# Performance work log

Measured on AMD Instinct MI355X. Metric: run time of the kernel, lower is better.

The kernel has to match this reference:

```python
import jax, jax.numpy as jnp
import numpy as np

DEPTH = 6
HEADS = 8
DIM = 512
DH = DIM // HEADS          # 64
SEQ = 512
BATCH = 8
MEM = 4096                 # KNN memory slots per batch element (scaled from 64000)
TOPK = 32                  # num_retrieved_memories
KNN_LAYERS = (3, 4)        # memorizing_layers=(4,5), 1-indexed -> 0-indexed 3,4
FF = 4 * DIM


def setup_inputs() -> dict:
    key = jax.random.key(0)
    ks = jax.random.split(key, 18)
    s = 0.02
    return {
        "x":     jax.random.normal(ks[0], (BATCH, SEQ, DIM), jnp.float32),
        "Wq":    jax.random.normal(ks[1], (DEPTH, DIM, DIM), jnp.float32) * s,
        "Wk":    jax.random.normal(ks[2], (DEPTH, DIM, DIM), jnp.float32) * s,
        "Wv":    jax.random.normal(ks[3], (DEPTH, DIM, DIM), jnp.float32) * s,
        "Wo":    jax.random.normal(ks[4], (DEPTH, DIM, DIM), jnp.float32) * s,
        "ln1_s": jnp.ones((DEPTH, DIM), jnp.float32),
        "ln1_b": jnp.zeros((DEPTH, DIM), jnp.float32),
        "ln2_s": jnp.ones((DEPTH, DIM), jnp.float32),
        "ln2_b": jnp.zeros((DEPTH, DIM), jnp.float32),
        "W1":    jax.random.normal(ks[5], (DEPTH, DIM, FF), jnp.float32) * s,
        "W2":    jax.random.normal(ks[6], (DEPTH, FF, DIM), jnp.float32) * s,
        "lnf_s": jnp.ones((DIM,), jnp.float32),
        "lnf_b": jnp.zeros((DIM,), jnp.float32),
        # pre-populated KNN memory banks (keys/values in head dim), one per memorizing layer
        "mem_k": jax.random.normal(ks[7], (len(KNN_LAYERS), BATCH, MEM, DH), jnp.float32),
        "mem_v": jax.random.normal(ks[8], (len(KNN_LAYERS), BATCH, MEM, DH), jnp.float32),
    }


def _ln(x, s, b):
    m = x.mean(-1, keepdims=True)
    v = ((x - m) ** 2).mean(-1, keepdims=True)
    return (x - m) * jax.lax.rsqrt(v + 1e-5) * s + b


def _gather_mem(mem, idx):
    # mem: (b, M, d), idx: (b, h, n, K) -> (b, h, n, K, d)
    return jax.vmap(lambda m, i: m[i])(mem, idx)


def reference(x, Wq, Wk, Wv, Wo, ln1_s, ln1_b, ln2_s, ln2_b, W1, W2,
              lnf_s, lnf_b, mem_k, mem_v):
    b, n, d = x.shape
    scale = DH ** -0.5
    causal = jnp.tril(jnp.ones((n, n), dtype=bool))
    neg = jnp.float32(-1e9)
    mem_i = 0
    for l in range(DEPTH):
        h = _ln(x, ln1_s[l], ln1_b[l])
        q = (h @ Wq[l]).reshape(b, n, HEADS, DH)
        k = (h @ Wk[l]).reshape(b, n, HEADS, DH)
        v = (h @ Wv[l]).reshape(b, n, HEADS, DH)
        sim = jnp.einsum('bihd,bjhd->bhij', q, k) * scale
        sim = jnp.where(causal, sim, neg)
        if l in KNN_LAYERS:
            mk, mv = mem_k[mem_i], mem_v[mem_i]              # (b, M, dh)
            # KNN search: dense scoring + top-k retrieval
            sim_all = jnp.einsum('bihd,bmd->bhim', q, mk) * scale  # (b,h,n,M)
            top_sim, top_idx = jax.lax.top_k(sim_all, TOPK)        # (b,h,n,K)
            gv = _gather_mem(mv, top_idx)                          # (b,h,n,K,dh)
            # joint softmax over [retrieved memories, local causal]
            logits = jnp.concatenate([top_sim, sim], axis=-1)
            attn = jax.nn.softmax(logits, axis=-1)
            a_mem, a_loc = attn[..., :TOPK], attn[..., TOPK:]
            out = (jnp.einsum('bhik,bhikd->bhid', a_mem, gv)
                   + jnp.einsum('bhij,bjhd->bhid', a_loc, v))
            mem_i += 1
        else:
            attn = jax.nn.softmax(sim, axis=-1)
            out = jnp.einsum('bhij,bjhd->bhid', attn, v)
        out = out.transpose(0, 2, 1, 3).reshape(b, n, d) @ Wo[l]
        x = x + out
        h2 = _ln(x, ln2_s[l], ln2_b[l])
        x = x + jax.nn.gelu(h2 @ W1[l]) @ W2[l]
    return _ln(x, lnf_s, lnf_b)
```

## Files before the change

kernel.cpp:

```cpp
#include <hip/hip_runtime.h>
#include <math.h>

#define BB 8
#define NN 512
#define DD 512
#define HH 8
#define DHH 64
#define FFF 2048
#define MEMM 4096
#define TOPKK 32
#define DEPTHH 6
#define NT (BB*NN)
#define QKVS 1536

typedef __bf16 bf16x8 __attribute__((ext_vector_type(8)));
typedef __bf16 bf16x4 __attribute__((ext_vector_type(4)));
typedef float f32x4 __attribute__((ext_vector_type(4)));

template <int OBF16>
__global__ __launch_bounds__(256) void ln_kernel(const float* __restrict__ xin,
                                                 const float* __restrict__ g,
                                                 const float* __restrict__ bt,
                                                 void* __restrict__ outv) {
  __shared__ float red[4];
  int tok = blockIdx.x;
  const float* xr = xin + (size_t)tok * DD;
  int t = threadIdx.x;
  float v0 = xr[t], v1 = xr[t + 256];
  float s = v0 + v1;
#pragma unroll
  for (int m = 32; m; m >>= 1) s += __shfl_xor(s, m, 64);
  if ((t & 63) == 0) red[t >> 6] = s;
  __syncthreads();
  float mean = (red[0] + red[1] + red[2] + red[3]) * (1.0f / 512.0f);
  float d0 = v0 - mean, d1 = v1 - mean;
  float vv = d0 * d0 + d1 * d1;
#pragma unroll
  for (int m = 32; m; m >>= 1) vv += __shfl_xor(vv, m, 64);
  __syncthreads();
  if ((t & 63) == 0) red[t >> 6] = vv;
  __syncthreads();
  float var = (red[0] + red[1] + red[2] + red[3]) * (1.0f / 512.0f);
  float inv = rsqrtf(var + 1e-5f);
  float o0 = d0 * inv * g[t] + bt[t];
  float o1 = d1 * inv * g[t + 256] + bt[t + 256];
  if (OBF16) {
    __bf16* out = (__bf16*)outv;
    out[(size_t)tok * DD + t] = (__bf16)o0;
    out[(size_t)tok * DD + t + 256] = (__bf16)o1;
  } else {
    float* out = (float*)outv;
    out[(size_t)tok * DD + t] = o0;
    out[(size_t)tok * DD + t + 256] = o1;
  }
}

__device__ inline float gelu_f(float x) {
  float x3 = x * x * x;
  return 0.5f * x * (1.0f + tanhf(0.7978845608028654f * (x + 0.044715f * x3)));
}

__global__ __launch_bounds__(256) void transpose_all_kernel(
    const float* __restrict__ Wq, const float* __restrict__ Wk,
    const float* __restrict__ Wv, const float* __restrict__ Wo,
    const float* __restrict__ W1, const float* __restrict__ W2,
    __bf16* __restrict__ wqT, __bf16* __restrict__ wkT,
    __bf16* __restrict__ wvT, __bf16* __restrict__ woT,
    __bf16* __restrict__ w1T, __bf16* __restrict__ w2T) {
  __shared__ float tile[32][33];
  int tid = blockIdx.x;
  const float* src; __bf16* dst; int K, N, tt;
  if (tid < 1024) {
    int which = tid >> 8; tt = tid & 255; K = 512; N = 512;
    src = (which == 0) ? Wq : (which == 1) ? Wk : (which == 2) ? Wv : Wo;
    dst = (which == 0) ? wqT : (which == 1) ? wkT : (which == 2) ? wvT : woT;
  } else if (tid < 2048) {
    tt = tid - 1024; K = 512; N = 2048; src = W1; dst = w1T;
  } else {
    tt = tid - 2048; K = 2048; N = 512; src = W2; dst = w2T;
  }
  int nx = N >> 5;
  int n0 = (tt % nx) * 32, k0 = (tt / nx) * 32;
  int tx = threadIdx.x & 31, ty = threadIdx.x >> 5;
#pragma unroll
  for (int i = 0; i < 4; i++) {
    int r = ty + i * 8;
    tile[r][tx] = src[(size_t)(k0 + r) * N + n0 + tx];
  }
  __syncthreads();
#pragma unroll
  for (int i = 0; i < 4; i++) {
    int r = ty + i * 8;
    dst[(size_t)(n0 + r) * K + k0 + tx] = (__bf16)tile[tx][r];
  }
}

__device__ __forceinline__ void gload16(const __bf16* g, __bf16* lds) {
  __builtin_amdgcn_global_load_lds(
      (const __attribute__((address_space(1))) void*)g,
      (__attribute__((address_space(3))) void*)lds, 16, 0, 0);
}

template <int EPI, int OBF16>
__global__ __launch_bounds__(256) void gemm_mfma128(const __bf16* __restrict__ A,
                                                    const __bf16* __restrict__ Bt,
                                                    const float* __restrict__ R,
                                                    void* __restrict__ Cout,
                                                    int M, int N, int K) {
  __shared__ __align__(16) __bf16 Als[128 * 64];
  __shared__ __align__(16) __bf16 Bls[128 * 64];
  int t = threadIdx.x;
  int bn = blockIdx.x, bm = blockIdx.y;
  int lane = t & 63, w = t >> 6;
  int wr = w >> 1, wc = w & 1;
  int m15 = lane & 15, q = lane >> 4;
  f32x4 acc[4][4] = {};
  for (int kt = 0; kt < K; kt += 64) {
    __syncthreads();
#pragma unroll
    for (int i = 0; i < 4; i++) {
      int rg = w * 32 + i * 8;
      int row = rg + (lane >> 3);
      int lcol = (lane & 7) * 8;
      gload16(A + (size_t)(bm * 128 + row) * K + kt + lcol, &Als[rg * 64]);
      gload16(Bt + (size_t)(bn * 128 + row) * K + kt + lcol, &Bls[rg * 64]);
    }
    __syncthreads();
#pragma unroll
    for (int ks = 0; ks < 2; ks++) {
      bf16x8 af[4], bfr[4];
#pragma unroll
      for (int mt = 0; mt < 4; mt++)
        af[mt] = *(const bf16x8*)&Als[(wr * 64 + mt * 16 + m15) * 64 + (ks * 4 + q) * 8];
#pragma unroll
      for (int nt = 0; nt < 4; nt++)
        bfr[nt] = *(const bf16x8*)&Bls[(wc * 64 + nt * 16 + m15) * 64 + (ks * 4 + q) * 8];
#pragma unroll
      for (int mt = 0; mt < 4; mt++)
#pragma unroll
        for (int nt = 0; nt < 4; nt++)
          acc[mt][nt] = __builtin_amdgcn_mfma_f32_16x16x32_bf16(af[mt], bfr[nt],
                                                                acc[mt][nt], 0, 0, 0);
    }
  }
#pragma unroll
  for (int mt = 0; mt < 4; mt++) {
#pragma unroll
    for (int nt = 0; nt < 4; nt++) {
      int gc = bn * 128 + wc * 64 + nt * 16 + m15;
#pragma unroll
      for (int r = 0; r < 4; r++) {
        int gr = bm * 128 + wr * 64 + mt * 16 + q * 4 + r;
        size_t off = (size_t)gr * N + gc;
        float v = acc[mt][nt][r];
        if (EPI == 1) v = gelu_f(v);
        if (EPI == 2) v += R[off];
        if (OBF16) ((__bf16*)Cout)[off] = (__bf16)v;
        else       ((float*)Cout)[off] = v;
      }
    }
  }
}

template <int EPI, int OBF16>
__global__ __launch_bounds__(256) void gemm_mfma64(const __bf16* __restrict__ A,
                                                   const __bf16* __restrict__ Bt,
                                                   const float* __restrict__ R,
                                                   void* __restrict__ Cout,
                                                   int M, int N, int K) {
  __shared__ __align__(16) __bf16 Als[128 * 64];
  __shared__ __align__(16) __bf16 Bls[64 * 64];
  int t = threadIdx.x;
  int bn = blockIdx.x, bm = blockIdx.y;
  int lane = t & 63, w = t >> 6;
  int wr = w >> 1, wc = w & 1;
  int m15 = lane & 15, q = lane >> 4;
  f32x4 acc[4][2] = {};
  for (int kt = 0; kt < K; kt += 64) {
    __syncthreads();
#pragma unroll
    for (int i = 0; i < 4; i++) {
      int rg = w * 32 + i * 8;
      int row = rg + (lane >> 3);
      int lcol = (lane & 7) * 8;
      gload16(A + (size_t)(bm * 128 + row) * K + kt + lcol, &Als[rg * 64]);
    }
#pragma unroll
    for (int i = 0; i < 2; i++) {
      int rg = w * 16 + i * 8;
      int row = rg + (lane >> 3);
      int lcol = (lane & 7) * 8;
      gload16(Bt + (size_t)(bn * 64 + row) * K + kt + lcol, &Bls[rg * 64]);
    }
    __syncthreads();
#pragma unroll
    for (int ks = 0; ks < 2; ks++) {
      bf16x8 af[4], bfr[2];
#pragma unroll
      for (int mt = 0; mt < 4; mt++)
        af[mt] = *(const bf16x8*)&Als[(wr * 64 + mt * 16 + m15) * 64 + (ks * 4 + q) * 8];
#pragma unroll
      for (int nt = 0; nt < 2; nt++)
        bfr[nt] = *(const bf16x8*)&Bls[(wc * 32 + nt * 16 + m15) * 64 + (ks * 4 + q) * 8];
#pragma unroll
      for (int mt = 0; mt < 4; mt++)
#pragma unroll
        for (int nt = 0; nt < 2; nt++)
          acc[mt][nt] = __builtin_amdgcn_mfma_f32_16x16x32_bf16(af[mt], bfr[nt],
                                                                acc[mt][nt], 0, 0, 0);
    }
  }
#pragma unroll
  for (int mt = 0; mt < 4; mt++) {
#pragma unroll
    for (int nt = 0; nt < 2; nt++) {
      int gc = bn * 64 + wc * 32 + nt * 16 + m15;
#pragma unroll
      for (int r = 0; r < 4; r++) {
        int gr = bm * 128 + wr * 64 + mt * 16 + q * 4 + r;
        size_t off = (size_t)gr * N + gc;
        float v = acc[mt][nt][r];
        if (EPI == 1) v = gelu_f(v);
        if (EPI == 2) v += R[off];
        if (OBF16) ((__bf16*)Cout)[off] = (__bf16)v;
        else       ((float*)Cout)[off] = v;
      }
    }
  }
}

__global__ __launch_bounds__(256) void split_bf16_kernel(const float* __restrict__ src,
                                                         __bf16* __restrict__ hi,
                                                         __bf16* __restrict__ lo) {
  int i = blockIdx.x * 256 + threadIdx.x;
  float4 v = ((const float4*)src)[i];
  float xs[4] = {v.x, v.y, v.z, v.w};
  bf16x4 hv, lv;
#pragma unroll
  for (int e = 0; e < 4; e++) {
    __bf16 h = (__bf16)xs[e];
    hv[e] = h;
    lv[e] = (__bf16)(xs[e] - (float)h);
  }
  *(bf16x4*)&hi[(size_t)i * 4] = hv;
  *(bf16x4*)&lo[(size_t)i * 4] = lv;
}

__global__ __launch_bounds__(256) void vtrans_split_kernel(const float* __restrict__ qkv,
                                                           __bf16* __restrict__ vth,
                                                           __bf16* __restrict__ vtl) {
  __shared__ float tile[64 * 68];
  int tt = blockIdx.x, h = blockIdx.y, b = blockIdx.z;
  int t = threadIdx.x;
#pragma unroll
  for (int i = 0; i < 4; i++) {
    int lin = i * 256 + t, row = lin >> 4, c = (lin & 15) * 4;
    float4 x = *(const float4*)(qkv + ((size_t)(b * NN) + tt * 64 + row) * QKVS + 1024 + h * DHH + c);
    *(float4*)&tile[row * 68 + c] = x;
  }
  __syncthreads();
  int d = t >> 2, tb = (t & 3) * 16;
  float xs[16];
#pragma unroll
  for (int j = 0; j < 16; j++) xs[j] = tile[(tb + j) * 68 + d];
  bf16x8 h0, h1, l0, l1;
#pragma unroll
  for (int j = 0; j < 8; j++) {
    __bf16 a = (__bf16)xs[j];
    h0[j] = a; l0[j] = (__bf16)(xs[j] - (float)a);
    __bf16 bmv = (__bf16)xs[8 + j];
    h1[j] = bmv; l1[j] = (__bf16)(xs[8 + j] - (float)bmv);
  }
  size_t ob = ((size_t)(b * HH + h) * 64 + d) * NN + tt * 64 + tb;
  *(bf16x8*)(vth + ob) = h0; *(bf16x8*)(vth + ob + 8) = h1;
  *(bf16x8*)(vtl + ob) = l0; *(bf16x8*)(vtl + ob + 8) = l1;
}

#define MSPLIT 4
__global__ __launch_bounds__(256) void knn_score_mfma(const float* __restrict__ q,
                                                      const __bf16* __restrict__ khi,
                                                      const __bf16* __restrict__ klo,
                                                      __bf16* __restrict__ S,
                                                      int bh0) {
  __shared__ __bf16 Kls[2][128 * 72];
  int it = blockIdx.x, bh = bh0 + blockIdx.y;
  int mz = blockIdx.z;
  int b = bh >> 3, h = bh & 7;
  int t = threadIdx.x;
  int lane = t & 63, w = t >> 6;
  int m15 = lane & 15, kg = lane >> 4;
  const float scale = 0.125f;

  bf16x8 aqh[2][2], aql[2][2];
#pragma unroll
  for (int rf = 0; rf < 2; rf++)
#pragma unroll
    for (int ks = 0; ks < 2; ks++) {
      const float* qp = q + ((size_t)(b * NN) + it * 32 + rf * 16 + m15) * QKVS +
                        h * DHH + ks * 32 + kg * 8;
      float4 x0 = *(const float4*)qp;
      float4 x1 = *(const float4*)(qp + 4);
      float xs[8] = {x0.x, x0.y, x0.z, x0.w, x1.x, x1.y, x1.z, x1.w};
#pragma unroll
      for (int e = 0; e < 8; e++) {
        __bf16 hv = (__bf16)xs[e];
        aqh[rf][ks][e] = hv;
        aql[rf][ks][e] = (__bf16)(xs[e] - (float)hv);
      }
    }

  const __bf16* khb = khi + (size_t)b * MEMM * DHH;
  const __bf16* klb = klo + (size_t)b * MEMM * DHH;
  size_t srow0 = (size_t)blockIdx.y * NN + it * 32;

  const int mlo = mz * (MEMM / MSPLIT), mhi = mlo + MEMM / MSPLIT;
  for (int mt = mlo; mt < mhi; mt += 128) {
    __syncthreads();
#pragma unroll
    for (int i = 0; i < 4; i++) {
      int lin = i * 256 + t;
      int row = lin >> 3, cb = (lin & 7) * 8;
      *(uint4*)&Kls[0][row * 72 + cb] = *(const uint4*)(khb + (size_t)(mt + row) * DHH + cb);
      *(uint4*)&Kls[1][row * 72 + cb] = *(const uint4*)(klb + (size_t)(mt + row) * DHH + cb);
    }
    __syncthreads();
    f32x4 acc[2][2] = {};
#pragma unroll
    for (int ks = 0; ks < 2; ks++) {
      bf16x8 bh2[2], bl2[2];
#pragma unroll
      for (int cf = 0; cf < 2; cf++) {
        int row = w * 32 + cf * 16 + m15;
        bh2[cf] = *(const bf16x8*)&Kls[0][row * 72 + ks * 32 + kg * 8];
        bl2[cf] = *(const bf16x8*)&Kls[1][row * 72 + ks * 32 + kg * 8];
      }
#pragma unroll
      for (int rf = 0; rf < 2; rf++)
#pragma unroll
        for (int cf = 0; cf < 2; cf++) {
          acc[rf][cf] = __builtin_amdgcn_mfma_f32_16x16x32_bf16(aqh[rf][ks], bh2[cf], acc[rf][cf], 0, 0, 0);
          acc[rf][cf] = __builtin_amdgcn_mfma_f32_16x16x32_bf16(aql[rf][ks], bh2[cf], acc[rf][cf], 0, 0, 0);
          acc[rf][cf] = __builtin_amdgcn_mfma_f32_16x16x32_bf16(aqh[rf][ks], bl2[cf], acc[rf][cf], 0, 0, 0);
        }
    }
#pragma unroll
    for (int rf = 0; rf < 2; rf++)
#pragma unroll
      for (int cf = 0; cf < 2; cf++) {
        int col = mt + w * 32 + cf * 16 + m15;
#pragma unroll
        for (int rr = 0; rr < 4; rr++)
          S[(srow0 + rf * 16 + kg * 4 + rr) * MEMM + col] = (__bf16)(acc[rf][cf][rr] * scale);
      }
  }
}

__global__ __launch_bounds__(256, 4) void knn_select_kernel(const __bf16* __restrict__ S,
                                                            float* __restrict__ topv,
                                                            int* __restrict__ topi,
                                                            int row_base) {
  int lane = threadIdx.x & 63;
  int row = blockIdx.x * 4 + (threadIdx.x >> 6);
  const __bf16* srow = S + (size_t)row * MEMM;
  unsigned u[64];
#pragma unroll
  for (int i = 0; i < 8; i++) {
    uint4 v = *(const uint4*)(srow + i * 512 + lane * 8);
    unsigned vs[4] = {v.x, v.y, v.z, v.w};
#pragma unroll
    for (int e2 = 0; e2 < 4; e2++) {
      unsigned lo = vs[e2] & 0xffffu, hi2 = vs[e2] >> 16;
      u[i * 8 + e2 * 2 + 0] = (lo & 0x8000u) ? (~lo & 0xffffu) : (lo | 0x8000u);
      u[i * 8 + e2 * 2 + 1] = (hi2 & 0x8000u) ? (~hi2 & 0xffffu) : (hi2 | 0x8000u);
    }
  }
  unsigned T = 0;
#pragma unroll 1
  for (int bit = 15; bit >= 0; --bit) {
    unsigned Tp = T | (1u << bit);
    int c = 0;
#pragma unroll
    for (int j = 0; j < 64; j++) c += (u[j] >= Tp) ? 1 : 0;
#pragma unroll
    for (int m = 32; m; m >>= 1) c += __shfl_xor(c, m, 64);
    if (c >= TOPKK) {
      T = Tp;
      if (c == TOPKK) break;
    }
  }
  unsigned long long below = (1ull << lane) - 1ull;
  float* tvrow = topv + (size_t)(row_base + row) * TOPKK;
  int* tirow = topi + (size_t)(row_base + row) * TOPKK;
  int g = 0;
#pragma unroll
  for (int i = 0; i < 8; i++)
#pragma unroll
    for (int e = 0; e < 8; e++) {
      int j = i * 8 + e;
      bool f = u[j] > T;
      unsigned long long m = __ballot(f);
      if (f) {
        int pos = g + __popcll(m & below);
        unsigned b16 = (u[j] & 0x8000u) ? (u[j] & 0x7fffu) : (~u[j] & 0xffffu);
        union { unsigned b; float f2; } rv; rv.b = b16 << 16;
        tvrow[pos] = rv.f2;
        tirow[pos] = i * 512 + lane * 8 + e;
      }
      g += __popcll(m);
    }
#pragma unroll 1
  for (int i = 0; i < 8 && g < TOPKK; i++)
#pragma unroll
    for (int e = 0; e < 8; e++) {
      int j = i * 8 + e;
      bool f = (u[j] == T);
      unsigned long long m = __ballot(f);
      if (f) {
        int pos = g + __popcll(m & below);
        if (pos < TOPKK) {
          unsigned b16 = (T & 0x8000u) ? (T & 0x7fffu) : (~T & 0xffffu);
          union { unsigned b; float f2; } rv; rv.b = b16 << 16;
          tvrow[pos] = rv.f2;
          tirow[pos] = i * 512 + lane * 8 + e;
        }
      }
      g += __popcll(m);
    }
}

__device__ __forceinline__ void insert32vi(float (&rtv)[32], int (&rti)[32],
                                           float sv, int idx, float& thr) {
  float mv = rtv[0], mv2 = INFINITY;
  int mi = 0;
#pragma unroll
  for (int k = 1; k < 32; k++) {
    float v = rtv[k];
    bool lt = v < mv;
    mv2 = lt ? mv : fminf(mv2, v);
    mv = lt ? v : mv;
    mi = lt ? k : mi;
  }
#pragma unroll
  for (int k = 0; k < 32; k++) {
    bool hit = (k == mi);
    rtv[k] = hit ? sv : rtv[k];
    rti[k] = hit ? idx : rti[k];
  }
  thr = fminf(mv2, sv);
}

__global__ __launch_bounds__(256) void knn_mfma_topk(const float* __restrict__ q,
                                                     const __bf16* __restrict__ khi,
                                                     const __bf16* __restrict__ klo,
                                                     float* __restrict__ topv,
                                                     int* __restrict__ topi) {
  __shared__ __bf16 Kls[2][128 * 72];
  __shared__ float scb[32][132];
  __shared__ unsigned short midx[32 * 260];
  __shared__ float rthr[8][32];
  int it = blockIdx.x, h = blockIdx.y, b = blockIdx.z;
  int t = threadIdx.x;
  int lane = t & 63, w = t >> 6;
  int m15 = lane & 15, kg = lane >> 4;
  const float scale = 0.125f;
  bf16x8 aqh[2][2], aql[2][2];
#pragma unroll
  for (int rf = 0; rf < 2; rf++)
#pragma unroll
    for (int ks = 0; ks < 2; ks++) {
      const float* qp = q + ((size_t)(b * NN) + it * 32 + rf * 16 + m15) * QKVS +
                        h * DHH + ks * 32 + kg * 8;
      float4 x0 = *(const float4*)qp;
      float4 x1 = *(const float4*)(qp + 4);
      float xs[8] = {x0.x, x0.y, x0.z, x0.w, x1.x, x1.y, x1.z, x1.w};
#pragma unroll
      for (int e = 0; e < 8; e++) {
        __bf16 hv = (__bf16)xs[e];
        aqh[rf][ks][e] = hv;
        aql[rf][ks][e] = (__bf16)(xs[e] - (float)hv);
      }
    }
  int r = t & 31, p = t >> 5;
  rthr[p][r] = -INFINITY;
  float rtv[32]; int rti[32];
#pragma unroll
  for (int k = 0; k < 32; k++) { rtv[k] = -INFINITY; rti[k] = 0; }
  float thr = -INFINITY;
  const __bf16* khb = khi + (size_t)b * MEMM * DHH;
  const __bf16* klb = klo + (size_t)b * MEMM * DHH;

  for (int mt = 0; mt < MEMM; mt += 128) {
    __syncthreads();
#pragma unroll
    for (int i = 0; i < 4; i++) {
      int lin = i * 256 + t;
      int row = lin >> 3, cb = (lin & 7) * 8;
      *(uint4*)&Kls[0][row * 72 + cb] = *(const uint4*)(khb + (size_t)(mt + row) * DHH + cb);
      *(uint4*)&Kls[1][row * 72 + cb] = *(const uint4*)(klb + (size_t)(mt + row) * DHH + cb);
    }
    __syncthreads();
    f32x4 acc[2][2] = {};
#pragma unroll
    for (int ks = 0; ks < 2; ks++) {
      bf16x8 bh2[2], bl2[2];
#pragma unroll
      for (int cf = 0; cf < 2; cf++) {
        int row = w * 32 + cf * 16 + m15;
        bh2[cf] = *(const bf16x8*)&Kls[0][row * 72 + ks * 32 + kg * 8];
        bl2[cf] = *(const bf16x8*)&Kls[1][row * 72 + ks * 32 + kg * 8];
      }
#pragma unroll
      for (int rf = 0; rf < 2; rf++)
#pragma unroll
        for (int cf = 0; cf < 2; cf++) {
          acc[rf][cf] = __builtin_amdgcn_mfma_f32_16x16x32_bf16(aqh[rf][ks], bh2[cf], acc[rf][cf], 0, 0, 0);
          acc[rf][cf] = __builtin_amdgcn_mfma_f32_16x16x32_bf16(aql[rf][ks], bh2[cf], acc[rf][cf], 0, 0, 0);
          acc[rf][cf] = __builtin_amdgcn_mfma_f32_16x16x32_bf16(aqh[rf][ks], bl2[cf], acc[rf][cf], 0, 0, 0);
        }
    }
#pragma unroll
    for (int rf = 0; rf < 2; rf++)
#pragma unroll
      for (int cf = 0; cf < 2; cf++) {
        int col = w * 32 + cf * 16 + m15;
#pragma unroll
        for (int rr = 0; rr < 4; rr++)
          scb[rf * 16 + kg * 4 + rr][col] = acc[rf][cf][rr] * scale;
      }
    __syncthreads();
    {
      float B2 = rthr[0][r];
#pragma unroll
      for (int j = 1; j < 8; j++) B2 = fmaxf(B2, rthr[j][r]);
      const float* srow = &scb[r][16 * p];
#pragma unroll 1
      for (int c = 0; c < 16; c++) {
        int cc = (c + r) & 15;
        float sv = srow[cc];
        if (sv > fmaxf(thr, B2))
          insert32vi(rtv, rti, sv, mt + 16 * p + cc, thr);
      }
      rthr[p][r] = thr;
    }
  }
  __syncthreads();
  float* mvals = (float*)&Kls[0][0];
#pragma unroll
  for (int k = 0; k < 32; k++) {
    int cc = (k + r) & 31;
    mvals[(size_t)260 * r + 32 * p + cc] = rtv[k];
    midx[(size_t)260 * r + 32 * p + cc] = (unsigned short)rti[k];
  }
  __syncthreads();
  if (t < 32) {
#pragma unroll 1
    for (int c = 0; c < 224; c++) {
      int cc = c + r; if (cc >= 224) cc -= 224;
      float sv = mvals[(size_t)260 * r + 32 + cc];
      if (sv > thr)
        insert32vi(rtv, rti, sv, (int)midx[(size_t)260 * r + 32 + cc], thr);
    }
    size_t rowg = ((size_t)b * HH + h) * NN + it * 32 + r;
#pragma unroll
    for (int k = 0; k < 32; k++) {
      topv[rowg * TOPKK + k] = rtv[k];
      topi[rowg * TOPKK + k] = rti[k];
    }
  }
}

__global__ __launch_bounds__(256) void attn_mfma_kernel(
    const float* __restrict__ qkv,
    const __bf16* __restrict__ vth, const __bf16* __restrict__ vtl,
    __bf16* __restrict__ ao, const float* __restrict__ topv,
    const int* __restrict__ topi, const float* __restrict__ mem_v, int knn) {
  __shared__ __align__(16) __bf16 smem[27648];
  __bf16* Kh = smem;
  __bf16* Kl = smem + 4608;
  __bf16* Vh = smem + 9216;
  __bf16* Vl = smem + 13824;
  __bf16* Pw = smem + 18432;

  int flat = blockIdx.x;
  int bi = flat >> 6;
  int hb = flat & 63;
  int h = hb & 7, b = hb >> 3;
  int t = threadIdx.x, lane = t & 63, w = t >> 6;
  int q15 = lane & 15, g = lane >> 4;
  const float scale = 0.125f;

  bf16x8 qh[2], ql[2];
  {
    const float* qp = qkv + ((size_t)(b * NN) + bi * 64 + w * 16 + q15) * QKVS + h * DHH;
#pragma unroll
    for (int ks = 0; ks < 2; ks++) {
      float4 x0 = *(const float4*)(qp + ks * 32 + g * 8);
      float4 x1 = *(const float4*)(qp + ks * 32 + g * 8 + 4);
      float xs[8] = {x0.x, x0.y, x0.z, x0.w, x1.x, x1.y, x1.z, x1.w};
#pragma unroll
      for (int e = 0; e < 8; e++) {
        __bf16 hv = (__bf16)xs[e];
        qh[ks][e] = hv;
        ql[ks][e] = (__bf16)(xs[e] - (float)hv);
      }
    }
  }
  int tr = t >> 4, kc = (t & 15) * 4;
  int td = t >> 3, tb = (t & 7) * 8;
  float4 kp0, kp1, kp2, kp3;
  uint4 vhp0, vhp1, vlp0, vlp1;

#define LOAD_TILE(jt_) do {                                                        \
    const float* kb_ = qkv + ((size_t)(b * NN) + (jt_) * 64 + tr) * QKVS + 512 +   \
                       h * DHH + kc;                                               \
    kp0 = *(const float4*)kb_;                                                     \
    kp1 = *(const float4*)(kb_ + (size_t)16 * QKVS);                               \
    kp2 = *(const float4*)(kb_ + (size_t)32 * QKVS);                               \
    kp3 = *(const float4*)(kb_ + (size_t)48 * QKVS);                               \
    size_t vb_ = ((size_t)(b * HH + h) * 64 + td) * NN + (jt_) * 64 + tb;          \
    vhp0 = *(const uint4*)(vth + vb_);                                             \
    vhp1 = *(const uint4*)(vth + vb_ + (size_t)32 * NN);                           \
    vlp0 = *(const uint4*)(vtl + vb_);                                             \
    vlp1 = *(const uint4*)(vtl + vb_ + (size_t)32 * NN);                           \
  } while (0)

#define STORE_K(kp_, ro_) do {                                                     \
    bf16x4 hv_, lv_;                                                               \
    float e0_ = kp_.x, e1_ = kp_.y, e2_ = kp_.z, e3_ = kp_.w;                      \
    hv_[0] = (__bf16)e0_; lv_[0] = (__bf16)(e0_ - (float)hv_[0]);                  \
    hv_[1] = (__bf16)e1_; lv_[1] = (__bf16)(e1_ - (float)hv_[1]);                  \
    hv_[2] = (__bf16)e2_; lv_[2] = (__bf16)(e2_ - (float)hv_[2]);                  \
    hv_[3] = (__bf16)e3_; lv_[3] = (__bf16)(e3_ - (float)hv_[3]);                  \
    *(bf16x4*)&Kh[((ro_) + tr) * 72 + kc] = hv_;                                   \
    *(bf16x4*)&Kl[((ro_) + tr) * 72 + kc] = lv_;                                   \
  } while (0)

  float m_run = -INFINITY, l_run = 0.f;
  f32x4 opv[4] = {};
  int ntiles = bi + 1;
  LOAD_TILE(0);
  for (int jt = 0; jt < ntiles; jt++) {
    __syncthreads();
    STORE_K(kp0, 0); STORE_K(kp1, 16); STORE_K(kp2, 32); STORE_K(kp3, 48);
    *(uint4*)&Vh[td * 72 + tb] = vhp0;
    *(uint4*)&Vh[(32 + td) * 72 + tb] = vhp1;
    *(uint4*)&Vl[td * 72 + tb] = vlp0;
    *(uint4*)&Vl[(32 + td) * 72 + tb] = vlp1;
    if (jt + 1 < ntiles) LOAD_TILE(jt + 1);
    __syncthreads();
    int smax = (jt == bi) ? w : 3;
    float sc16[16];
    float tmax = -INFINITY;
#pragma unroll
    for (int s = 0; s < 4; s++) {
      if (s <= smax) {
        f32x4 accs = {};
#pragma unroll
        for (int ks = 0; ks < 2; ks++) {
          bf16x8 ah = *(const bf16x8*)&Kh[(s * 16 + q15) * 72 + ks * 32 + g * 8];
          bf16x8 al = *(const bf16x8*)&Kl[(s * 16 + q15) * 72 + ks * 32 + g * 8];
          accs = __builtin_amdgcn_mfma_f32_16x16x32_bf16(ah, qh[ks], accs, 0, 0, 0);
          accs = __builtin_amdgcn_mfma_f32_16x16x32_bf16(al, qh[ks], accs, 0, 0, 0);
          accs = __builtin_amdgcn_mfma_f32_16x16x32_bf16(ah, ql[ks], accs, 0, 0, 0);
        }
#pragma unroll
        for (int r = 0; r < 4; r++) {
          float sv = accs[r] * scale;
          if (jt == bi) {
            int kvg = jt * 64 + s * 16 + g * 4 + r;
            int qg = bi * 64 + w * 16 + q15;
            if (kvg > qg) sv = -INFINITY;
          }
          sc16[s * 4 + r] = sv;
          tmax = fmaxf(tmax, sv);
        }
      } else {
#pragma unroll
        for (int r = 0; r < 4; r++) sc16[s * 4 + r] = -INFINITY;
      }
    }
    tmax = fmaxf(tmax, __shfl_xor(tmax, 16, 64));
    tmax = fmaxf(tmax, __shfl_xor(tmax, 32, 64));
    float m_new = fmaxf(m_run, tmax);
    float psum = 0.f;
    __bf16 ph[16], pl[16];
#pragma unroll
    for (int i = 0; i < 16; i++) {
      float p = __expf(sc16[i] - m_new);
      psum += p;
      __bf16 hp = (__bf16)p;
      ph[i] = hp; pl[i] = (__bf16)(p - (float)hp);
    }
    psum += __shfl_xor(psum, 16, 64);
    psum += __shfl_xor(psum, 32, 64);
    float alpha = __expf(m_run - m_new);
    l_run = l_run * alpha + psum;
    m_run = m_new;
    __bf16* Ph = Pw + (w * 2 + 0) * 1152;
    __bf16* Pl = Pw + (w * 2 + 1) * 1152;
#pragma unroll
    for (int s = 0; s < 4; s++) {
      bf16x4 hv, lv;
#pragma unroll
      for (int r = 0; r < 4; r++) { hv[r] = ph[s * 4 + r]; lv[r] = pl[s * 4 + r]; }
      *(bf16x4*)&Ph[q15 * 72 + s * 16 + g * 4] = hv;
      *(bf16x4*)&Pl[q15 * 72 + s * 16 + g * 4] = lv;
    }
    __builtin_amdgcn_wave_barrier();
    float a0 = __shfl(alpha, g * 4 + 0, 64);
    float a1 = __shfl(alpha, g * 4 + 1, 64);
    float a2 = __shfl(alpha, g * 4 + 2, 64);
    float a3 = __shfl(alpha, g * 4 + 3, 64);
#pragma unroll
    for (int dsub = 0; dsub < 4; dsub++) {
      opv[dsub][0] *= a0; opv[dsub][1] *= a1;
      opv[dsub][2] *= a2; opv[dsub][3] *= a3;
    }
#pragma unroll
    for (int ks2 = 0; ks2 < 2; ks2++) {
      bf16x8 pah = *(const bf16x8*)&Ph[q15 * 72 + ks2 * 32 + g * 8];
      bf16x8 pal = *(const bf16x8*)&Pl[q15 * 72 + ks2 * 32 + g * 8];
#pragma unroll
      for (int dsub = 0; dsub < 4; dsub++) {
        bf16x8 vbh = *(const bf16x8*)&Vh[(dsub * 16 + q15) * 72 + ks2 * 32 + g * 8];
        bf16x8 vbl = *(const bf16x8*)&Vl[(dsub * 16 + q15) * 72 + ks2 * 32 + g * 8];
        opv[dsub] = __builtin_amdgcn_mfma_f32_16x16x32_bf16(pah, vbh, opv[dsub], 0, 0, 0);
        opv[dsub] = __builtin_amdgcn_mfma_f32_16x16x32_bf16(pal, vbh, opv[dsub], 0, 0, 0);
        opv[dsub] = __builtin_amdgcn_mfma_f32_16x16x32_bf16(pah, vbl, opv[dsub], 0, 0, 0);
      }
    }
  }
#undef LOAD_TILE
#undef STORE_K
  __syncthreads();
  float* scf  = (float*)smem;
  float* marr = (float*)(smem + 8704);
  float* larr = marr + 64;
  float* aarr = marr + 128;
  float* sc2  = (float*)(smem + 9216);
  int*   pidx = (int*)(smem + 13824);
#pragma unroll
  for (int dsub = 0; dsub < 4; dsub++)
#pragma unroll
    for (int r = 0; r < 4; r++)
      scf[(w * 16 + g * 4 + r) * 68 + dsub * 16 + q15] = opv[dsub][r];
  if (g == 0) { marr[w * 16 + q15] = m_run; larr[w * 16 + q15] = l_run; }
  __syncthreads();
  int r_ = t & 63, w4 = t >> 6;
  float acc16[16];
  if (knn) {
    size_t rowbase = ((size_t)b * HH + h) * NN + bi * 64;
    for (int rr = w * 16; rr < w * 16 + 16; rr++) {
      float s = (lane < TOPKK) ? topv[(rowbase + rr) * TOPKK + lane] : -INFINITY;
      float m_old = marr[rr];
      float tm = s;
#pragma unroll
      for (int m = 32; m; m >>= 1) tm = fmaxf(tm, __shfl_xor(tm, m, 64));
      float m_new = fmaxf(m_old, tm);
      float p = __expf(s - m_new);
      float ts = p;
#pragma unroll
      for (int m = 32; m; m >>= 1) ts += __shfl_xor(ts, m, 64);
      float alpha = __expf(m_old - m_new);
      if (lane < TOPKK) {
        sc2[rr * 33 + lane] = p;
        pidx[rr * 32 + lane] = topi[(rowbase + rr) * TOPKK + lane];
      }
      if (lane == 0) {
        marr[rr] = m_new; larr[rr] = larr[rr] * alpha + ts; aarr[rr] = alpha;
      }
    }
    __syncthreads();
    float al = aarr[r_];
#pragma unroll
    for (int dd = 0; dd < 16; dd++) acc16[dd] = scf[r_ * 68 + w4 * 16 + dd] * al;
    const float* mvb = mem_v + (size_t)b * MEMM * DHH;
#pragma unroll 1
    for (int kk = 0; kk < TOPKK; kk++) {
      float p = sc2[r_ * 33 + kk];
      const float* mrow = mvb + (size_t)pidx[r_ * 32 + kk] * DHH + w4 * 16;
#pragma unroll
      for (int dd = 0; dd < 16; dd += 4) {
        float4 m4 = *(const float4*)(mrow + dd);
        acc16[dd] += p * m4.x; acc16[dd + 1] += p * m4.y;
        acc16[dd + 2] += p * m4.z; acc16[dd + 3] += p * m4.w;
      }
    }
  } else {
#pragma unroll
    for (int dd = 0; dd < 16; dd++) acc16[dd] = scf[r_ * 68 + w4 * 16 + dd];
  }
  float linv = 1.f / larr[r_];
  bf16x8 o0, o1;
#pragma unroll
  for (int j = 0; j < 8; j++) {
    o0[j] = (__bf16)(acc16[j] * linv);
    o1[j] = (__bf16)(acc16[8 + j] * linv);
  }
  __bf16* aop = ao + ((size_t)(b * NN) + bi * 64 + r_) * DD + h * DHH + w4 * 16;
  *(bf16x8*)aop = o0;
  *(bf16x8*)(aop + 8) = o1;
}

extern "C" void kernel_launch(void* const* d_in, const int* in_sizes, int n_in,
                              void* d_out, int out_size, void* d_ws, size_t ws_size,
                              hipStream_t stream) {
  const float* x_in  = (const float*)d_in[0];
  const float* Wq    = (const float*)d_in[1];
  const float* Wk    = (const float*)d_in[2];
  const float* Wv    = (const float*)d_in[3];
  const float* Wo    = (const float*)d_in[4];
  const float* ln1_s = (const float*)d_in[5];
  const float* ln1_b = (const float*)d_in[6];
  const float* ln2_s = (const float*)d_in[7];
  const float* ln2_b = (const float*)d_in[8];
  const float* W1    = (const float*)d_in[9];
  const float* W2    = (const float*)d_in[10];
  const float* lnf_s = (const float*)d_in[11];
  const float* lnf_b = (const float*)d_in[12];
  const float* mem_k = (const float*)d_in[13];
  const float* mem_v = (const float*)d_in[14];

  float* ws  = (float*)d_ws;
  float*  xb    = ws;
  float*  qkvb  = ws + 2097152;
  __bf16* hb16  = (__bf16*)(ws + 8388608);
  __bf16* ao16  = (__bf16*)(ws + 9437184);
  __bf16* wqT   = (__bf16*)(ws + 10485760);
  __bf16* woT   = (__bf16*)(ws + 10878976);
  __bf16* w1T   = (__bf16*)(ws + 11010048);
  __bf16* w2T   = (__bf16*)(ws + 11534336);
  float*  tvb   = ws + 12058624;
  int*    tib   = (int*)(ws + 13107200);
  __bf16* ffb16 = (__bf16*)(ws + 2097152);
  __bf16* wkT   = wqT + 262144;
  __bf16* wvT   = wqT + 524288;
  __bf16* khi16 = (__bf16*)(ws + 8388608);
  __bf16* klo16 = (__bf16*)(ws + 9437184);

  const size_t base_floats = 14155776;
  const size_t slice_floats = (size_t)NN * MEMM;
  const size_t ws_floats = ws_size / sizeof(float);
  int nbh = 0;
  for (int c = 64; c >= 1; c >>= 1) {
    if (base_floats + (size_t)c * slice_floats <= ws_floats) { nbh = c; break; }
  }
  __bf16* Sb16 = (__bf16*)(ws + base_floats);
  __bf16* vth = (__bf16*)(ws + base_floats);
  __bf16* vtl = (__bf16*)(ws + base_floats + 1048576);

  dim3 blk(256);
  const size_t DD2 = (size_t)DD * DD;
  for (int l = 0; l < DEPTHH; l++) {
    const float* xcur = (l == 0) ? x_in : xb;
    transpose_all_kernel<<<dim3(3072), blk, 0, stream>>>(
        Wq + l * DD2, Wk + l * DD2, Wv + l * DD2, Wo + l * DD2,
        W1 + (size_t)l * DD * FFF, W2 + (size_t)l * FFF * DD,
        wqT, wkT, wvT, woT, w1T, w2T);

    ln_kernel<1><<<NT, blk, 0, stream>>>(xcur, ln1_s + l * DD, ln1_b + l * DD, hb16);
    gemm_mfma64<0, 0><<<dim3(24, 32), blk, 0, stream>>>(hb16, wqT, nullptr, qkvb, NT, QKVS, DD);
    int mi = (l == 3) ? 0 : ((l == 4) ? 1 : -1);
    if (mi >= 0) {
      const float* mk = mem_k + (size_t)mi * BB * MEMM * DHH;
      split_bf16_kernel<<<dim3(BB * MEMM * DHH / 1024), blk, 0, stream>>>(mk, khi16, klo16);
      if (nbh > 0) {
        for (int bh0 = 0; bh0 < BB * HH; bh0 += nbh) {
          knn_score_mfma<<<dim3(16, nbh, MSPLIT), blk, 0, stream>>>(qkvb, khi16, klo16, Sb16, bh0);
          knn_select_kernel<<<dim3(nbh * NN / 4), blk, 0, stream>>>(Sb16, tvb, tib, bh0 * NN);
        }
      } else {
        knn_mfma_topk<<<dim3(16, 8, 8), blk, 0, stream>>>(qkvb, khi16, klo16, tvb, tib);
      }
    }
    vtrans_split_kernel<<<dim3(8, 8, 8), blk, 0, stream>>>(qkvb, vth, vtl);
    attn_mfma_kernel<<<dim3(512), blk, 0, stream>>>(
        qkvb, vth, vtl, ao16, tvb, tib,
        mem_v + (size_t)(mi < 0 ? 0 : mi) * BB * MEMM * DHH, mi >= 0 ? 1 : 0);
    gemm_mfma64<2, 0><<<dim3(8, 32), blk, 0, stream>>>(ao16, woT, xcur, xb, NT, DD, DD);
    ln_kernel<1><<<NT, blk, 0, stream>>>(xb, ln2_s + l * DD, ln2_b + l * DD, hb16);
    gemm_mfma128<1, 1><<<dim3(16, 32), blk, 0, stream>>>(hb16, w1T, nullptr, ffb16, NT, FFF, DD);
    gemm_mfma64<2, 0><<<dim3(8, 32), blk, 0, stream>>>(ffb16, w2T, xb, xb, NT, DD, FFF);
  }
  ln_kernel<0><<<NT, blk, 0, stream>>>(xb, lnf_s, lnf_b, (float*)d_out);
}
```

Before: 1.898 ms.

## Fuse KNN scoring with per-strip top-k selection and add a merge pass

Replaces the write-the-full-score-matrix-then-select scheme with a fused kernel. Each block scores a 512-column memory strip into shared memory, radix-selects a local top-32 per query row, and writes only those candidates. A small merge kernel then picks the final top-32 from the 8 strips' 256 candidates per row. The aim is to drop the large bf16 score-matrix round trip through global memory and the per-chunk launch loop, at the cost of extra shared memory per block and a second selection pass.

```diff
diff --git a/kernel.cpp b/kernel.cpp
--- a/kernel.cpp
+++ b/kernel.cpp
@@ -12,6 +12,8 @@
 #define DEPTHH 6
 #define NT (BB*NN)
 #define QKVS 1536
+#define NSTRIP 8
+#define STRIPC 512
 
 typedef __bf16 bf16x8 __attribute__((ext_vector_type(8)));
 typedef __bf16 bf16x4 __attribute__((ext_vector_type(4)));
@@ -276,15 +278,13 @@
   *(bf16x8*)(vtl + ob) = l0; *(bf16x8*)(vtl + ob + 8) = l1;
 }
 
-#define MSPLIT 4
-__global__ __launch_bounds__(256) void knn_score_mfma(const float* __restrict__ q,
-                                                      const __bf16* __restrict__ khi,
-                                                      const __bf16* __restrict__ klo,
-                                                      __bf16* __restrict__ S,
-                                                      int bh0) {
+__global__ __launch_bounds__(256) void knn_score_select(
+    const float* __restrict__ q, const __bf16* __restrict__ khi,
+    const __bf16* __restrict__ klo, float* __restrict__ locv,
+    int* __restrict__ loci) {
   __shared__ __bf16 Kls[2][128 * 72];
-  int it = blockIdx.x, bh = bh0 + blockIdx.y;
-  int mz = blockIdx.z;
+  __shared__ __align__(16) __bf16 Sls[32][520];
+  int it = blockIdx.x, bh = blockIdx.y, st = blockIdx.z;
   int b = bh >> 3, h = bh & 7;
   int t = threadIdx.x;
   int lane = t & 63, w = t >> 6;
@@ -311,10 +311,10 @@
 
   const __bf16* khb = khi + (size_t)b * MEMM * DHH;
   const __bf16* klb = klo + (size_t)b * MEMM * DHH;
-  size_t srow0 = (size_t)blockIdx.y * NN + it * 32;
-
-  const int mlo = mz * (MEMM / MSPLIT), mhi = mlo + MEMM / MSPLIT;
-  for (int mt = mlo; mt < mhi; mt += 128) {
+  const int m0 = st * STRIPC;
+
+  for (int tt = 0; tt < STRIPC; tt += 128) {
+    int mt = m0 + tt;
     __syncthreads();
 #pragma unroll
     for (int i = 0; i < 4; i++) {
@@ -347,72 +347,56 @@
     for (int rf = 0; rf < 2; rf++)
 #pragma unroll
       for (int cf = 0; cf < 2; cf++) {
-        int col = mt + w * 32 + cf * 16 + m15;
+        int col = tt + w * 32 + cf * 16 + m15;
 #pragma unroll
         for (int rr = 0; rr < 4; rr++)
-          S[(srow0 + rf * 16 + kg * 4 + rr) * MEMM + col] = (__bf16)(acc[rf][cf][rr] * scale);
-      }
-  }
-}
-
-__global__ __launch_bounds__(256, 4) void knn_select_kernel(const __bf16* __restrict__ S,
-                                                            float* __restrict__ topv,
-                                                            int* __restrict__ topi,
-                                                            int row_base) {
-  int lane = threadIdx.x & 63;
-  int row = blockIdx.x * 4 + (threadIdx.x >> 6);
-  const __bf16* srow = S + (size_t)row * MEMM;
-  unsigned u[64];
-#pragma unroll
-  for (int i = 0; i < 8; i++) {
-    uint4 v = *(const uint4*)(srow + i * 512 + lane * 8);
+          Sls[rf * 16 + kg * 4 + rr][col] = (__bf16)(acc[rf][cf][rr] * scale);
+      }
+  }
+  __syncthreads();
+
+  unsigned long long below = (1ull << lane) - 1ull;
+  for (int rl = w * 8; rl < w * 8 + 8; rl++) {
+    uint4 v = *(const uint4*)&Sls[rl][lane * 8];
     unsigned vs[4] = {v.x, v.y, v.z, v.w};
+    unsigned u[8];
 #pragma unroll
     for (int e2 = 0; e2 < 4; e2++) {
       unsigned lo = vs[e2] & 0xffffu, hi2 = vs[e2] >> 16;
-      u[i * 8 + e2 * 2 + 0] = (lo & 0x8000u) ? (~lo & 0xffffu) : (lo | 0x8000u);
-      u[i * 8 + e2 * 2 + 1] = (hi2 & 0x8000u) ? (~hi2 & 0xffffu) : (hi2 | 0x8000u);
-    }
-  }
-  unsigned T = 0;
+      u[e2 * 2 + 0] = (lo & 0x8000u) ? (~lo & 0xffffu) : (lo | 0x8000u);
+      u[e2 * 2 + 1] = (hi2 & 0x8000u) ? (~hi2 & 0xffffu) : (hi2 | 0x8000u);
+    }
+    unsigned T = 0;
 #pragma unroll 1
-  for (int bit = 15; bit >= 0; --bit) {
-    unsigned Tp = T | (1u << bit);
-    int c = 0;
-#pragma unroll
-    for (int j = 0; j < 64; j++) c += (u[j] >= Tp) ? 1 : 0;
-#pragma unroll
-    for (int m = 32; m; m >>= 1) c += __shfl_xor(c, m, 64);
-    if (c >= TOPKK) {
-      T = Tp;
-      if (c == TOPKK) break;
-    }
-  }
-  unsigned long long below = (1ull << lane) - 1ull;
-  float* tvrow = topv + (size_t)(row_base + row) * TOPKK;
-  int* tirow = topi + (size_t)(row_base + row) * TOPKK;
-  int g = 0;
-#pragma unroll
-  for (int i = 0; i < 8; i++)
-#pragma unroll
-    for (int e = 0; e < 8; e++) {
-      int j = i * 8 + e;
+    for (int bit = 15; bit >= 0; --bit) {
+      unsigned Tp = T | (1u << bit);
+      int c = 0;
+#pragma unroll
+      for (int j = 0; j < 8; j++) c += (u[j] >= Tp) ? 1 : 0;
+#pragma unroll
+      for (int m = 32; m; m >>= 1) c += __shfl_xor(c, m, 64);
+      if (c >= TOPKK) {
+        T = Tp;
+        if (c == TOPKK) break;
+      }
+    }
+    size_t obase = (((size_t)bh * NN + it * 32 + rl) * NSTRIP + st) * TOPKK;
+    int g = 0;
+#pragma unroll
+    for (int j = 0; j < 8; j++) {
       bool f = u[j] > T;
       unsigned long long m = __ballot(f);
       if (f) {
         int pos = g + __popcll(m & below);
         unsigned b16 = (u[j] & 0x8000u) ? (u[j] & 0x7fffu) : (~u[j] & 0xffffu);
         union { unsigned b; float f2; } rv; rv.b = b16 << 16;
-        tvrow[pos] = rv.f2;
-        tirow[pos] = i * 512 + lane * 8 + e;
+        locv[obase + pos] = rv.f2;
+        loci[obase + pos] = m0 + lane * 8 + j;
       }
       g += __popcll(m);
     }
 #pragma unroll 1
-  for (int i = 0; i < 8 && g < TOPKK; i++)
-#pragma unroll
-    for (int e = 0; e < 8; e++) {
-      int j = i * 8 + e;
+    for (int j = 0; j < 8 && g < TOPKK; j++) {
       bool f = (u[j] == T);
       unsigned long long m = __ballot(f);
       if (f) {
@@ -420,12 +404,76 @@
         if (pos < TOPKK) {
           unsigned b16 = (T & 0x8000u) ? (T & 0x7fffu) : (~T & 0xffffu);
           union { unsigned b; float f2; } rv; rv.b = b16 << 16;
-          tvrow[pos] = rv.f2;
-          tirow[pos] = i * 512 + lane * 8 + e;
+          locv[obase + pos] = rv.f2;
+          loci[obase + pos] = m0 + lane * 8 + j;
         }
       }
       g += __popcll(m);
     }
+  }
+}
+
+__global__ __launch_bounds__(256, 4) void knn_merge_kernel(
+    const float* __restrict__ locv, const int* __restrict__ loci,
+    float* __restrict__ topv, int* __restrict__ topi) {
+  int lane = threadIdx.x & 63;
+  int row = blockIdx.x * 4 + (threadIdx.x >> 6);
+  const float* lv = locv + (size_t)row * (NSTRIP * TOPKK);
+  const int* li = loci + (size_t)row * (NSTRIP * TOPKK);
+  uint4 vv = *(const uint4*)(lv + lane * 4);
+  uint4 vi = *(const uint4*)(li + lane * 4);
+  unsigned vs[4] = {vv.x, vv.y, vv.z, vv.w};
+  unsigned is[4] = {vi.x, vi.y, vi.z, vi.w};
+  unsigned u[4];
+#pragma unroll
+  for (int e = 0; e < 4; e++) {
+    unsigned hb = vs[e] >> 16;
+    u[e] = (hb & 0x8000u) ? (~hb & 0xffffu) : (hb | 0x8000u);
+  }
+  unsigned T = 0;
+#pragma unroll 1
+  for (int bit = 15; bit >= 0; --bit) {
+    unsigned Tp = T | (1u << bit);
+    int c = 0;
+#pragma unroll
+    for (int j = 0; j < 4; j++) c += (u[j] >= Tp) ? 1 : 0;
+#pragma unroll
+    for (int m = 32; m; m >>= 1) c += __shfl_xor(c, m, 64);
+    if (c >= TOPKK) {
+      T = Tp;
+      if (c == TOPKK) break;
+    }
+  }
+  unsigned long long below = (1ull << lane) - 1ull;
+  float* tvrow = topv + (size_t)row * TOPKK;
+  int* tirow = topi + (size_t)row * TOPKK;
+  int g = 0;
+#pragma unroll
+  for (int j = 0; j < 4; j++) {
+    bool f = u[j] > T;
+    unsigned long long m = __ballot(f);
+    if (f) {
+      int pos = g + __popcll(m & below);
+      union { unsigned b; float f2; } rv; rv.b = vs[j];
+      tvrow[pos] = rv.f2;
+      tirow[pos] = (int)is[j];
+    }
+    g += __popcll(m);
+  }
+#pragma unroll 1
+  for (int j = 0; j < 4 && g < TOPKK; j++) {
+    bool f = (u[j] == T);
+    unsigned long long m = __ballot(f);
+    if (f) {
+      int pos = g + __popcll(m & below);
+      if (pos < TOPKK) {
+        union { unsigned b; float f2; } rv; rv.b = vs[j];
+        tvrow[pos] = rv.f2;
+        tirow[pos] = (int)is[j];
+      }
+    }
+    g += __popcll(m);
+  }
 }
 
 __device__ __forceinline__ void insert32vi(float (&rtv)[32], int (&rti)[32],
@@ -839,13 +887,11 @@
   __bf16* klo16 = (__bf16*)(ws + 9437184);
 
   const size_t base_floats = 14155776;
-  const size_t slice_floats = (size_t)NN * MEMM;
+  const size_t loc_floats = (size_t)BB * HH * NN * NSTRIP * TOPKK;
   const size_t ws_floats = ws_size / sizeof(float);
-  int nbh = 0;
-  for (int c = 64; c >= 1; c >>= 1) {
-    if (base_floats + (size_t)c * slice_floats <= ws_floats) { nbh = c; break; }
-  }
-  __bf16* Sb16 = (__bf16*)(ws + base_floats);
+  bool bigws = base_floats + 2 * loc_floats <= ws_floats;
+  float* locv = ws + base_floats;
+  int*   loci = (int*)(ws + base_floats + loc_floats);
   __bf16* vth = (__bf16*)(ws + base_floats);
   __bf16* vtl = (__bf16*)(ws + base_floats + 1048576);
 
@@ -864,11 +910,10 @@
     if (mi >= 0) {
       const float* mk = mem_k + (size_t)mi * BB * MEMM * DHH;
       split_bf16_kernel<<<dim3(BB * MEMM * DHH / 1024), blk, 0, stream>>>(mk, khi16, klo16);
-      if (nbh > 0) {
-        for (int bh0 = 0; bh0 < BB * HH; bh0 += nbh) {
-          knn_score_mfma<<<dim3(16, nbh, MSPLIT), blk, 0, stream>>>(qkvb, khi16, klo16, Sb16, bh0);
-          knn_select_kernel<<<dim3(nbh * NN / 4), blk, 0, stream>>>(Sb16, tvb, tib, bh0 * NN);
-        }
+      if (bigws) {
+        knn_score_select<<<dim3(16, BB * HH, NSTRIP), blk, 0, stream>>>(
+            qkvb, khi16, klo16, locv, loci);
+        knn_merge_kernel<<<dim3(BB * HH * NN / 4), blk, 0, stream>>>(locv, loci, tvb, tib);
       } else {
         knn_mfma_topk<<<dim3(16, 8, 8), blk, 0, stream>>>(qkvb, khi16, klo16, tvb, tib);
       }
```

After: 2.700 ms. 42.3% more time.
